# Kernel tuning notes

Measured on AMD Instinct MI355X. Metric: run time of the kernel, lower is better.

The kernel has to match this reference:

```python
import jax, jax.numpy as jnp
import numpy as np

B, S, W = 128, 256, 1
DEPTH = 655            # MathTypeKeysMax
UNITS = 128
PROBLEM_BUCKETS = 32


def setup_inputs() -> dict:
    key = jax.random.key(0)
    ks = jax.random.split(key, 14)
    ri = lambda k, shape, hi: jax.random.randint(k, shape, 0, hi, dtype=jnp.int32)
    K = 4 * DEPTH * W  # flattened per-timestep feature width = 2620
    return {
        'move_count': ri(ks[0], (B,), 100),
        'moves_remaining': ri(ks[1], (B,), 100),
        'last_rule': ri(ks[2], (B,), 12),
        'node_count': ri(ks[3], (B,), 64),
        'problem_type': ri(ks[4], (B,), PROBLEM_BUCKETS),
        'bwd_vectors': ri(ks[5], (B, S, W), DEPTH),
        'fwd_vectors': ri(ks[6], (B, S, W), DEPTH),
        'last_bwd_vectors': ri(ks[7], (B, S, W), DEPTH),
        'last_fwd_vectors': ri(ks[8], (B, S, W), DEPTH),
        'W_dense': jax.random.normal(ks[9], (K, UNITS), jnp.float32) * (1.0 / np.sqrt(K)),
        'b_dense': jnp.zeros((UNITS,), jnp.float32),
        'Wx': jax.random.normal(ks[10], (UNITS, 4 * UNITS), jnp.float32) * (1.0 / np.sqrt(UNITS)),
        'Wh': jax.random.normal(ks[11], (UNITS, 4 * UNITS), jnp.float32) * (1.0 / np.sqrt(UNITS)),
        'b_lstm': jnp.zeros((4 * UNITS,), jnp.float32),
    }


def _lstm(x, Wx, Wh, b):
    # x: [B, S, U] -> (seq hidden [B, S, U], final hidden [B, U]); keras gate order i,f,c,o
    U = Wh.shape[0]
    bsz = x.shape[0]
    # precompute input projections once: [S, B, 4U]
    xz = jnp.einsum('bsu,uv->sbv', x, Wx) + b

    def step(carry, zt):
        h, c = carry
        z = zt + h @ Wh
        i, f, g, o = jnp.split(z, 4, axis=-1)
        i = jax.nn.sigmoid(i)
        f = jax.nn.sigmoid(f)
        g = jnp.tanh(g)
        o = jax.nn.sigmoid(o)
        c = f * c + i * g
        h = o * jnp.tanh(c)
        return (h, c), h

    init = (jnp.zeros((bsz, U), x.dtype), jnp.zeros((bsz, U), x.dtype))
    (h_last, _), hs = jax.lax.scan(step, init, xz)
    return jnp.transpose(hs, (1, 0, 2)), h_last


def reference(move_count, moves_remaining, last_rule, node_count, problem_type,
              bwd_vectors, fwd_vectors, last_bwd_vectors, last_fwd_vectors,
              W_dense, b_dense, Wx, Wh, b_lstm):
    f32 = lambda a: a.astype(jnp.float32)
    # DenseFeatures context extraction: 3 numeric int columns + 32-bucket indicator
    context_inputs = jnp.concatenate([
        f32(last_rule)[:, None],
        f32(move_count)[:, None],
        f32(node_count)[:, None],
        jax.nn.one_hot(problem_type, PROBLEM_BUCKETS, dtype=jnp.float32),
    ], axis=-1)  # [B, 35]

    sequence_length = bwd_vectors.shape[1]
    # one-hot each [B,S,W] sequence to [B,S,W,DEPTH], concat on last axis -> [B,S,W,4*DEPTH]
    oh = jnp.concatenate([
        jax.nn.one_hot(bwd_vectors, DEPTH, dtype=jnp.float32),
        jax.nn.one_hot(fwd_vectors, DEPTH, dtype=jnp.float32),
        jax.nn.one_hot(last_bwd_vectors, DEPTH, dtype=jnp.float32),
        jax.nn.one_hot(last_fwd_vectors, DEPTH, dtype=jnp.float32),
    ], axis=-1)
    bsz = oh.shape[0]
    # per-example Flatten keeps leading S dim, so the loop == one batched matmul
    flat = oh.reshape(bsz, sequence_length, -1)      # [B, S, 4*DEPTH*W]
    outputs = jnp.einsum('bsk,ku->bsu', flat, W_dense) + b_dense  # [B, S, U]

    hidden_states, lstm_vectors = _lstm(outputs, Wx, Wh, b_lstm)
    return (context_inputs, lstm_vectors, hidden_states, sequence_length)
```

## Files before the change

kernel.cpp:

```cpp
#include <hip/hip_runtime.h>
#include <cstdint>

#define BB   128
#define SS   256
#define NDEPTH 655
#define UU   128
#define VV   512
#define NPB  32

__device__ __forceinline__ float sigm(float x) {
    return 1.0f / (1.0f + expf(-x));
}

__global__ void context_kernel(const int* __restrict__ last_rule,
                               const int* __restrict__ move_count,
                               const int* __restrict__ node_count,
                               const int* __restrict__ problem_type,
                               float* __restrict__ out, int write_seq) {
    int i = blockIdx.x * blockDim.x + threadIdx.x;
    if (i < BB * 35) {
        int b = i / 35, c = i % 35;
        float v;
        if (c == 0)      v = (float)last_rule[b];
        else if (c == 1) v = (float)move_count[b];
        else if (c == 2) v = (float)node_count[b];
        else             v = (problem_type[b] == (c - 3)) ? 1.0f : 0.0f;
        out[i] = v;
    }
    if (write_seq && i == 0)
        out[(size_t)BB*35 + (size_t)BB*UU + (size_t)BB*SS*UU] = (float)SS;
}

__global__ void wdwx_kernel(const float* __restrict__ Wd,
                            const float* __restrict__ Wx,
                            const float* __restrict__ b_dense,
                            const float* __restrict__ b_lstm,
                            float* __restrict__ WdWx,
                            float* __restrict__ base) {
    int v  = threadIdx.x;
    int k0 = blockIdx.x * 4;
    const float* wd0 = Wd + (size_t)k0 * UU;
    float a0 = 0.f, a1 = 0.f, a2 = 0.f, a3 = 0.f;
    for (int u = 0; u < UU; ++u) {
        float wx = Wx[u * VV + v];
        a0 = fmaf(wd0[u],        wx, a0);
        a1 = fmaf(wd0[UU + u],   wx, a1);
        a2 = fmaf(wd0[2*UU + u], wx, a2);
        a3 = fmaf(wd0[3*UU + u], wx, a3);
    }
    WdWx[(size_t)(k0+0)*VV + v] = a0;
    WdWx[(size_t)(k0+1)*VV + v] = a1;
    WdWx[(size_t)(k0+2)*VV + v] = a2;
    WdWx[(size_t)(k0+3)*VV + v] = a3;
    if (blockIdx.x == 0) {
        float a = 0.f;
        for (int u = 0; u < UU; ++u) a = fmaf(b_dense[u], Wx[u * VV + v], a);
        base[v] = a + b_lstm[v];
    }
}

__global__ __launch_bounds__(512, 2)
void lstm_kernel(const int* __restrict__ bwd,  const int* __restrict__ fwd,
                 const int* __restrict__ lbwd, const int* __restrict__ lfwd,
                 const float* __restrict__ WdWx,
                 const float* __restrict__ base,
                 const float* __restrict__ Wh,
                 float* __restrict__ hidden_states,
                 float* __restrict__ lstm_vectors) {
    const int b = blockIdx.x;
    const int t = threadIdx.x;

    __shared__ __align__(16) float h_lds[UU];
    __shared__ float act[VV];
    __shared__ int   idx_lds[SS][4];

    float wh[UU];
    #pragma unroll
    for (int u = 0; u < UU; ++u) wh[u] = Wh[u * VV + t];

    for (int s = t; s < SS; s += 512) {
        idx_lds[s][0] =            bwd [b*SS + s];
        idx_lds[s][1] =   NDEPTH + fwd [b*SS + s];
        idx_lds[s][2] = 2*NDEPTH + lbwd[b*SS + s];
        idx_lds[s][3] = 3*NDEPTH + lfwd[b*SS + s];
    }
    if (t < UU) h_lds[t] = 0.0f;
    float c  = 0.0f;
    float bb = base[t];
    __syncthreads();

    float p0 = WdWx[(size_t)idx_lds[0][0] * VV + t];
    float p1 = WdWx[(size_t)idx_lds[0][1] * VV + t];
    float p2 = WdWx[(size_t)idx_lds[0][2] * VV + t];
    float p3 = WdWx[(size_t)idx_lds[0][3] * VV + t];

    for (int s = 0; s < SS; ++s) {
        float z = bb + p0 + p1 + p2 + p3;
        if (s + 1 < SS) {
            p0 = WdWx[(size_t)idx_lds[s+1][0] * VV + t];
            p1 = WdWx[(size_t)idx_lds[s+1][1] * VV + t];
            p2 = WdWx[(size_t)idx_lds[s+1][2] * VV + t];
            p3 = WdWx[(size_t)idx_lds[s+1][3] * VV + t];
        }
        float z0 = 0.f, z1 = 0.f, z2 = 0.f, z3 = 0.f;
        #pragma unroll
        for (int u = 0; u < UU; u += 4) {
            float4 hv = *(const float4*)(h_lds + u);
            z0 = fmaf(hv.x, wh[u],   z0);
            z1 = fmaf(hv.y, wh[u+1], z1);
            z2 = fmaf(hv.z, wh[u+2], z2);
            z3 = fmaf(hv.w, wh[u+3], z3);
        }
        z += (z0 + z1) + (z2 + z3);

        act[t] = (t >= 2*UU && t < 3*UU) ? tanhf(z) : sigm(z);
        __syncthreads();

        if (t < UU) {
            float gi = act[t], gf = act[UU + t], gg = act[2*UU + t], go = act[3*UU + t];
            c = fmaf(gf, c, gi * gg);
            float h = go * tanhf(c);
            h_lds[t] = h;
            hidden_states[((size_t)b * SS + s) * UU + t] = h;
        }
        __syncthreads();
    }
    if (t < UU) lstm_vectors[(size_t)b * UU + t] = h_lds[t];
}

extern "C" void kernel_launch(void* const* d_in, const int* in_sizes, int n_in,
                              void* d_out, int out_size, void* d_ws, size_t ws_size,
                              hipStream_t stream) {
    const int* move_count   = (const int*)d_in[0];
    const int* last_rule    = (const int*)d_in[2];
    const int* node_count   = (const int*)d_in[3];
    const int* problem_type = (const int*)d_in[4];
    const int* bwd          = (const int*)d_in[5];
    const int* fwd          = (const int*)d_in[6];
    const int* lbwd         = (const int*)d_in[7];
    const int* lfwd         = (const int*)d_in[8];
    const float* Wd         = (const float*)d_in[9];
    const float* b_dense    = (const float*)d_in[10];
    const float* Wx         = (const float*)d_in[11];
    const float* Wh         = (const float*)d_in[12];
    const float* b_lstm     = (const float*)d_in[13];

    float* out  = (float*)d_out;
    float* WdWx = (float*)d_ws;
    float* base = WdWx + (size_t)(4 * NDEPTH) * VV;

    float* lstm_out = out + BB * 35;
    float* hs_out   = lstm_out + BB * UU;
    int write_seq = (out_size > BB*35 + BB*UU + BB*SS*UU) ? 1 : 0;

    context_kernel<<<(BB*35 + 255)/256, 256, 0, stream>>>(
        last_rule, move_count, node_count, problem_type, out, write_seq);
    wdwx_kernel<<<NDEPTH, VV, 0, stream>>>(Wd, Wx, b_dense, b_lstm, WdWx, base);
    lstm_kernel<<<BB, VV, 0, stream>>>(bwd, fwd, lbwd, lfwd, WdWx, base, Wh,
                                       hs_out, lstm_out);
}
```

Before: 334.8 us.

## Split LSTM recurrent dot product across thread pairs and use fast transcendentals

The LSTM kernel now launches 1024 threads per batch row, with two threads per gate column. Each thread holds half of that column's Wh weights (64 registers instead of 128) and gathers two of the four input projections, and the pair combines partial sums with a shuffle. Sigmoid and tanh switch to __expf/__fdividef forms. The aim is to halve the serial recurrent FMA chain and register pressure per step, at the cost of an extra shuffle, a larger block with heavier barrier cost, and slightly lower transcendental accuracy.

```diff
diff --git a/kernel.cpp b/kernel.cpp
--- a/kernel.cpp
+++ b/kernel.cpp
@@ -8,8 +8,12 @@
 #define VV   512
 #define NPB  32
 
-__device__ __forceinline__ float sigm(float x) {
-    return 1.0f / (1.0f + expf(-x));
+__device__ __forceinline__ float sigm_fast(float x) {
+    return __fdividef(1.0f, 1.0f + __expf(-x));
+}
+__device__ __forceinline__ float tanh_fast(float x) {
+    float e = __expf(2.0f * x);
+    return 1.0f - __fdividef(2.0f, e + 1.0f);
 }
 
 __global__ void context_kernel(const int* __restrict__ last_rule,
@@ -59,7 +63,7 @@
     }
 }
 
-__global__ __launch_bounds__(512, 2)
+__global__ __launch_bounds__(1024, 4)
 void lstm_kernel(const int* __restrict__ bwd,  const int* __restrict__ fwd,
                  const int* __restrict__ lbwd, const int* __restrict__ lfwd,
                  const float* __restrict__ WdWx,
@@ -67,59 +71,61 @@
                  const float* __restrict__ Wh,
                  float* __restrict__ hidden_states,
                  float* __restrict__ lstm_vectors) {
-    const int b = blockIdx.x;
-    const int t = threadIdx.x;
+    const int b   = blockIdx.x;
+    const int t   = threadIdx.x;
+    const int col = t >> 1;
+    const int eps = t & 1;
 
     __shared__ __align__(16) float h_lds[UU];
     __shared__ float act[VV];
     __shared__ int   idx_lds[SS][4];
 
-    float wh[UU];
+    float wh[64];
+    const int u0 = eps * 64;
     #pragma unroll
-    for (int u = 0; u < UU; ++u) wh[u] = Wh[u * VV + t];
+    for (int u = 0; u < 64; ++u) wh[u] = Wh[(u0 + u) * VV + col];
 
-    for (int s = t; s < SS; s += 512) {
+    for (int s = t; s < SS; s += 1024) {
         idx_lds[s][0] =            bwd [b*SS + s];
         idx_lds[s][1] =   NDEPTH + fwd [b*SS + s];
         idx_lds[s][2] = 2*NDEPTH + lbwd[b*SS + s];
         idx_lds[s][3] = 3*NDEPTH + lfwd[b*SS + s];
     }
     if (t < UU) h_lds[t] = 0.0f;
-    float c  = 0.0f;
-    float bb = base[t];
+    float c    = 0.0f;
+    float bias = base[col];
     __syncthreads();
 
-    float p0 = WdWx[(size_t)idx_lds[0][0] * VV + t];
-    float p1 = WdWx[(size_t)idx_lds[0][1] * VV + t];
-    float p2 = WdWx[(size_t)idx_lds[0][2] * VV + t];
-    float p3 = WdWx[(size_t)idx_lds[0][3] * VV + t];
+    float p0 = WdWx[(size_t)idx_lds[0][2*eps    ] * VV + col];
+    float p1 = WdWx[(size_t)idx_lds[0][2*eps + 1] * VV + col];
 
     for (int s = 0; s < SS; ++s) {
-        float z = bb + p0 + p1 + p2 + p3;
+        float zp = (eps ? 0.0f : bias) + p0 + p1;
         if (s + 1 < SS) {
-            p0 = WdWx[(size_t)idx_lds[s+1][0] * VV + t];
-            p1 = WdWx[(size_t)idx_lds[s+1][1] * VV + t];
-            p2 = WdWx[(size_t)idx_lds[s+1][2] * VV + t];
-            p3 = WdWx[(size_t)idx_lds[s+1][3] * VV + t];
+            p0 = WdWx[(size_t)idx_lds[s+1][2*eps    ] * VV + col];
+            p1 = WdWx[(size_t)idx_lds[s+1][2*eps + 1] * VV + col];
         }
+        const float* hb = h_lds + u0;
         float z0 = 0.f, z1 = 0.f, z2 = 0.f, z3 = 0.f;
         #pragma unroll
-        for (int u = 0; u < UU; u += 4) {
-            float4 hv = *(const float4*)(h_lds + u);
+        for (int u = 0; u < 64; u += 4) {
+            float4 hv = *(const float4*)(hb + u);
             z0 = fmaf(hv.x, wh[u],   z0);
             z1 = fmaf(hv.y, wh[u+1], z1);
             z2 = fmaf(hv.z, wh[u+2], z2);
             z3 = fmaf(hv.w, wh[u+3], z3);
         }
-        z += (z0 + z1) + (z2 + z3);
+        zp += (z0 + z1) + (z2 + z3);
+        zp += __shfl_xor(zp, 1);
 
-        act[t] = (t >= 2*UU && t < 3*UU) ? tanhf(z) : sigm(z);
+        float a = (col >= 2*UU && col < 3*UU) ? tanh_fast(zp) : sigm_fast(zp);
+        act[col] = a;
         __syncthreads();
 
         if (t < UU) {
             float gi = act[t], gf = act[UU + t], gg = act[2*UU + t], go = act[3*UU + t];
             c = fmaf(gf, c, gi * gg);
-            float h = go * tanhf(c);
+            float h = go * tanh_fast(c);
             h_lds[t] = h;
             hidden_states[((size_t)b * SS + s) * UU + t] = h;
         }
@@ -156,6 +162,6 @@
     context_kernel<<<(BB*35 + 255)/256, 256, 0, stream>>>(
         last_rule, move_count, node_count, problem_type, out, write_seq);
     wdwx_kernel<<<NDEPTH, VV, 0, stream>>>(Wd, Wx, b_dense, b_lstm, WdWx, base);
-    lstm_kernel<<<BB, VV, 0, stream>>>(bwd, fwd, lbwd, lfwd, WdWx, base, Wh,
-                                       hs_out, lstm_out);
+    lstm_kernel<<<BB, 1024, 0, stream>>>(bwd, fwd, lbwd, lfwd, WdWx, base, Wh,
+                                         hs_out, lstm_out);
 }
```

Result: slower. 436.5 us (+30.4%).
